# Performance work log

Measured on AMD Instinct MI355X. Metric: run time of the kernel, lower is better.

The kernel has to match this reference:

```python
import jax, jax.numpy as jnp
import numpy as np

N_OSC = 2          # oscillators per group
GROUPS = 64        # channels // n_oscillators
EPS_GN = 1e-5      # GroupNorm eps (torch default)
EPS_NORM = 1e-12   # F.normalize clamp (torch default)


def setup_inputs() -> dict:
    key = jax.random.key(0)
    k0, k1, k2 = jax.random.split(key, 3)
    B, C, H, W = 8, 128, 96, 96
    KS = 7
    return {
        "x": jax.random.normal(k0, (B, C, H, W), jnp.float32),
        "c": jax.random.normal(k1, (B, C, H, W), jnp.float32),
        "conv_w": jax.random.normal(k2, (C, C, KS, KS), jnp.float32) * 0.02,
        "conv_b": jnp.zeros((C,), jnp.float32),
        "gn_w": jnp.ones((C,), jnp.float32),
        "gn_b": jnp.zeros((C,), jnp.float32),
        "omega": jnp.ones((1,), jnp.float32),
        "n_timesteps": 4,
    }


def _group_norm(c, w, b):
    B, C, H, W = c.shape
    cg = c.reshape(B, GROUPS, C // GROUPS, H, W)
    mu = cg.mean(axis=(2, 3, 4), keepdims=True)
    var = ((cg - mu) ** 2).mean(axis=(2, 3, 4), keepdims=True)
    cg = (cg - mu) * jax.lax.rsqrt(var + EPS_GN)
    return cg.reshape(B, C, H, W) * w[None, :, None, None] + b[None, :, None, None]


def _normalize_osc(x):
    # L2-normalize each group of N_OSC channels (unit-norm oscillators)
    B, C, H, W = x.shape
    xg = x.reshape(B, C // N_OSC, N_OSC, H, W)
    n = jnp.sqrt((xg * xg).sum(axis=2, keepdims=True))
    xg = xg / jnp.maximum(n, EPS_NORM)
    return xg.reshape(B, C, H, W)


def _conv(x, w, b):
    y = jax.lax.conv_general_dilated(
        x, w, window_strides=(1, 1), padding=[(3, 3), (3, 3)],
        dimension_numbers=("NCHW", "OIHW", "NCHW"))
    return y + b[None, :, None, None]


def _kuramoto_step(x, coupling, stim, omega, gamma):
    B, C, H, W = x.shape
    G = C // N_OSC
    y = coupling + stim                      # total drive
    xg = x.reshape(B, G, N_OSC, H, W)
    yg = y.reshape(B, G, N_OSC, H, W)
    # natural-frequency term: rotate each 2D oscillator pair by omega
    xp = xg.reshape(B, G, N_OSC // 2, 2, H, W)
    rot = jnp.stack([-xp[:, :, :, 1], xp[:, :, :, 0]], axis=3)
    omega_term = omega * rot.reshape(B, G, N_OSC, H, W)
    # project drive onto tangent space of the unit sphere per group
    inner = (xg * yg).sum(axis=2, keepdims=True)
    proj = yg - inner * xg
    x_new = _normalize_osc((xg + gamma * (omega_term + proj)).reshape(B, C, H, W))
    energy = -(y * x).sum(axis=(1, 2, 3))    # per-sample Kuramoto energy
    return x_new, energy


def reference(x, c, conv_w, conv_b, gn_w, gn_b, omega, n_timesteps):
    gamma = 1.0
    B = x.shape[0]
    c = _group_norm(c, gn_w, gn_b)
    x = _normalize_osc(x)
    om = omega.squeeze()
    xs = []
    es = [jnp.zeros((B,), x.dtype)]
    for _ in range(int(n_timesteps)):
        coupling = _conv(x, conv_w, conv_b)
        x, e = _kuramoto_step(x, coupling, c, om, gamma)
        xs.append(x)
        es.append(e)
    return jnp.stack(xs), jnp.stack(es)
```

## Files before the change

### kernel.cpp

```cpp
#include <hip/hip_runtime.h>
#include <math.h>

typedef unsigned short u16;
typedef unsigned int   u32;
typedef unsigned char  u8;
typedef __attribute__((ext_vector_type(4))) float f32x4;
typedef __attribute__((ext_vector_type(4))) u32   u32x4;
typedef __attribute__((ext_vector_type(8))) int   i32x8;
typedef __attribute__((ext_vector_type(4))) int   i32x4;

#define IMG_W 96
#define IMG_H 96
#define HWSZ  9216
#define CCH   128
#define BATCH 8
#define NT    4

#define PADW  102
#define PADA  (102*102)
#define XQ_BYTES ((size_t)BATCH*PADA*128)

#define XS_ELEMS (BATCH*CCH*HWSZ)
#define ES_OFF   (4*XS_ELEMS)

__device__ inline u16 f2bf(float f) {
    u32 u = __float_as_uint(f);
    u += 0x7fffu + ((u >> 16) & 1u);
    return (u16)(u >> 16);
}
__device__ inline float bf2f(u16 h) { return __uint_as_float(((u32)h) << 16); }

#define GLD_LDS16(g, l) \
    __builtin_amdgcn_global_load_lds((const __attribute__((address_space(1))) void*)(g), \
                                     (__attribute__((address_space(3))) void*)(l), 16, 0, 0)

__global__ __launch_bounds__(256) void gn_stats_kernel(
    const float* __restrict__ c, float* __restrict__ stats)
{
    const int bg  = blockIdx.x;
    const int tid = threadIdx.x;
    const float4* p4 = (const float4*)(c + (size_t)bg * 18432);
    float s1 = 0.f, s2 = 0.f;
    for (int i = tid; i < 18432/4; i += 256) {
        float4 v = p4[i];
        s1 += v.x + v.y + v.z + v.w;
        s2 += v.x*v.x + v.y*v.y + v.z*v.z + v.w*v.w;
    }
    __shared__ float r1[256], r2[256];
    r1[tid] = s1; r2[tid] = s2;
    __syncthreads();
    for (int s = 128; s > 0; s >>= 1) {
        if (tid < s) { r1[tid] += r1[tid+s]; r2[tid] += r2[tid+s]; }
        __syncthreads();
    }
    if (tid == 0) {
        float mu  = r1[0] * (1.f/18432.f);
        float var = fmaxf(r2[0] * (1.f/18432.f) - mu*mu, 0.f);
        stats[bg*2]   = mu;
        stats[bg*2+1] = rsqrtf(var + 1e-5f);
    }
}

__global__ __launch_bounds__(256) void wprep_kernel(
    const float* __restrict__ cw, u32* __restrict__ wq)
{
    int idx = blockIdx.x * 256 + threadIdx.x;
    if (idx >= 200704) return;
    int ic4 = idx & 31;
    int rem = idx >> 5;
    int oc  = rem & 127;
    int tap = rem >> 7;
    const float* s = cw + ((size_t)oc*128 + ic4*4)*49 + tap;
    float v0 = s[0], v1 = s[49], v2 = s[98], v3 = s[147];
    u32 lo = __builtin_amdgcn_cvt_pk_fp8_f32(v0, v1, 0, false);
    u32 pk = __builtin_amdgcn_cvt_pk_fp8_f32(v2, v3, lo, true);
    wq[(size_t)tap*4096 + oc*32 + ic4] = pk;
}

__global__ __launch_bounds__(256) void cprep_kernel(
    const float* __restrict__ c, const float* __restrict__ stats,
    const float* __restrict__ gnw, const float* __restrict__ gnb,
    const float* __restrict__ cb, u32* __restrict__ cgn)
{
    const int bg  = blockIdx.y;
    const int pix = blockIdx.x * 1024 + threadIdx.x * 4;
    const int b   = bg >> 6, g = bg & 63;
    const int ch0 = 2*g, ch1 = 2*g + 1;
    const float mu = stats[bg*2], rs = stats[bg*2+1];
    const float w0 = gnw[ch0]*rs, b0 = gnb[ch0] - mu*w0 + cb[ch0];
    const float w1 = gnw[ch1]*rs, b1 = gnb[ch1] - mu*w1 + cb[ch1];
    f32x4 c0 = *(const f32x4*)(c + ((size_t)(b*128+ch0))*HWSZ + pix);
    f32x4 c1 = *(const f32x4*)(c + ((size_t)(b*128+ch1))*HWSZ + pix);
    u32x4 v;
    #pragma unroll
    for (int j = 0; j < 4; ++j)
        v[j] = (u32)f2bf(fmaf(c0[j], w0, b0)) | ((u32)f2bf(fmaf(c1[j], w1, b1)) << 16);
    *(u32x4*)(cgn + (size_t)bg*HWSZ + pix) = v;
}

__global__ __launch_bounds__(256) void xprep_kernel(
    const float* __restrict__ x, u8* __restrict__ xq)
{
    __shared__ float s_t[128][65];
    const int b  = blockIdx.y;
    const int p0 = blockIdx.x * 64;
    const int tid = threadIdx.x;
    for (int it = 0; it < 32; ++it) {
        int idx = it*256 + tid;
        int ch = idx >> 6, p = idx & 63;
        s_t[ch][p] = x[((size_t)b*128 + ch)*HWSZ + p0 + p];
    }
    __syncthreads();
    for (int it = 0; it < 16; ++it) {
        int idx = it*256 + tid;
        int g = idx & 63, p = idx >> 6;
        int pix = p0 + p;
        int py = pix / 96, px = pix - py*96;
        float v0 = s_t[2*g][p], v1 = s_t[2*g+1][p];
        float sc = 1.f / fmaxf(sqrtf(v0*v0 + v1*v1), 1e-12f);
        u32 pk = __builtin_amdgcn_cvt_pk_fp8_f32(v0*sc, v1*sc, 0, false);
        *(u16*)(xq + ((size_t)b*PADA + (py+3)*PADW + (px+3))*128 + 2*g) = (u16)(pk & 0xffff);
    }
}

__global__ __launch_bounds__(384, 3) void convk8(
    const u8*    __restrict__ xq_in,
    const u8*    __restrict__ wq,
    const u32*   __restrict__ cgn,
    const float* __restrict__ omega,
    float* __restrict__ xout, u8* __restrict__ xq_out,
    float* __restrict__ es, int write_q)
{
    __shared__ __align__(16) u8 s_a[324*128];
    __shared__ __align__(16) u8 s_bb[2][16384];
    __shared__ float s_red[384];

    const int tid = threadIdx.x;
    const int w   = tid >> 6, l = tid & 63;
    const int b   = blockIdx.y;
    const int bx  = blockIdx.x;
    const int tpy = bx >> 3, tpx = bx & 7;
    const int wm  = w >> 1, wn = w & 1;
    const int l15 = l & 15, l4 = l >> 4;

    const u8* abase = xq_in + ((size_t)b*PADA + (size_t)tpy*12*PADW + (size_t)tpx*12)*128;

#define BARX { __builtin_amdgcn_sched_barrier(0); __builtin_amdgcn_s_barrier(); \
               __builtin_amdgcn_sched_barrier(0); }
#define WAITV0 { asm volatile("s_waitcnt vmcnt(0)" ::: "memory"); \
                 __builtin_amdgcn_sched_barrier(0); }

    #pragma unroll 1
    for (int it = 0; it < 7; ++it) {
        int i = it*384 + tid;
        if (i < 2592) {
            int p = i >> 3, g = i & 7;
            int hr = p / 18, hc = p - hr*18;
            int sxy = (4*hr + hc) & 7;
            const u8* src = abase + ((size_t)hr*PADW + hc)*128 + ((g ^ sxy) << 4);
            GLD_LDS16(src, s_a + i*16);
        }
    }

#define ISSUE_B(ksrc, dstbuf)                                              \
    { const u8* wsrc_ = wq + (size_t)(ksrc)*16384;                         \
      _Pragma("unroll")                                                    \
      for (int it_ = 0; it_ < 3; ++it_) {                                  \
          int i_ = (it_*384 + tid) & 1023;                                 \
          int oc_ = i_ >> 3, g_ = i_ & 7;                                  \
          GLD_LDS16(wsrc_ + oc_*128 + ((g_ ^ (oc_ & 7)) << 4),             \
                    (dstbuf) + i_*16);                                     \
      } }

    ISSUE_B(0, s_bb[0]);
    WAITV0;
    BARX;

    int pb[3], sbz[3];
    #pragma unroll
    for (int mi = 0; mi < 3; ++mi) {
        int m = wm*48 + mi*16 + l15;
        int pr = m/12, pc = m - pr*12;
        pb[mi]  = pr*18 + pc;
        sbz[mi] = (4*pr + pc) & 7;
    }
    int boff[4];
    #pragma unroll
    for (int ni = 0; ni < 4; ++ni) {
        int oc = wn*64 + ni*16 + l15;
        boff[ni] = oc*128 + (((l4*2) ^ (oc & 7)) << 4);
    }
    const int kloA = (l4*2) << 4;

#define READ_FRAGS(AF, BF, sbuf)                                           \
    { _Pragma("unroll")                                                    \
      for (int mi_ = 0; mi_ < 3; ++mi_) {                                  \
          int plin_ = pb[mi_] + pdN;                                       \
          int sx_   = ((sbz[mi_] + sdN) & 7) << 4;                         \
          const u8* base_ = s_a + plin_*128;                               \
          int a0_ = kloA ^ sx_;                                            \
          i32x4 lo_ = *(const i32x4*)(base_ + a0_);                        \
          i32x4 hi_ = *(const i32x4*)(base_ + (a0_ ^ 16));                 \
          AF[mi_] = __builtin_shufflevector(lo_, hi_, 0,1,2,3,4,5,6,7);    \
      }                                                                    \
      _Pragma("unroll")                                                    \
      for (int ni_ = 0; ni_ < 4; ++ni_) {                                  \
          i32x4 lo_ = *(const i32x4*)((sbuf) + boff[ni_]);                 \
          i32x4 hi_ = *(const i32x4*)((sbuf) + (boff[ni_] ^ 16));          \
          BF[ni_] = __builtin_shufflevector(lo_, hi_, 0,1,2,3,4,5,6,7);    \
      } }

#define DO_MFMA(AF, BF)                                                    \
    __builtin_amdgcn_s_setprio(1);                                         \
    _Pragma("unroll")                                                      \
    for (int mi_ = 0; mi_ < 3; ++mi_)                                      \
        _Pragma("unroll")                                                  \
        for (int ni_ = 0; ni_ < 4; ++ni_)                                  \
            acc[mi_][ni_] = __builtin_amdgcn_mfma_scale_f32_16x16x128_f8f6f4( \
                BF[ni_], AF[mi_], acc[mi_][ni_], 0, 0, 0, 0x7F, 0, 0x7F);  \
    __builtin_amdgcn_s_setprio(0);

#define ADV { if (++txc == 7) { txc = 0; pdN += 12; sdN = (sdN + 6) & 7; } \
              else            { ++pdN;  sdN = (sdN + 1) & 7; } }

    f32x4 acc[3][4] = {};
    i32x8 af[3], bfr[4];
    int pdN = 0, sdN = 0, txc = 0;
    int cur = 0;

    #pragma unroll 1
    for (int t = 0; t < 48; ++t) {
        READ_FRAGS(af, bfr, s_bb[cur]);
        ADV;
        ISSUE_B(t+1, s_bb[cur^1]);
        DO_MFMA(af, bfr);
        WAITV0;
        BARX;
        cur ^= 1;
    }
    READ_FRAGS(af, bfr, s_bb[cur]);
    DO_MFMA(af, bfr);

    const float om = omega[0];
    const size_t nb = (size_t)b * (CCH*HWSZ);
    float esum = 0.f;

    #pragma unroll
    for (int mi = 0; mi < 3; ++mi) {
        const int m   = wm*48 + mi*16 + l15;
        const int pr  = m/12, pc = m - pr*12;
        const int py  = tpy*12 + pr;
        const int px  = tpx*12 + pc;
        const int pixel = py*96 + px;
        const int hp  = (pr+3)*18 + (pc+3);
        const int hs  = (4*(pr+3) + (pc+3)) & 7;
        const u8* albase = s_a + hp*128;
        #pragma unroll
        for (int ni = 0; ni < 4; ++ni) {
            const int ocb = wn*64 + ni*16 + l4*4;
            float res[4];
            #pragma unroll
            for (int p2 = 0; p2 < 2; ++p2) {
                const int oc0 = ocb + p2*2;
                const int g   = oc0 >> 1;
                int goff = (((oc0 >> 4) ^ hs) << 4) + (oc0 & 15);
                int xv   = (int)*(const u16*)(albase + goff);
                float x0 = __builtin_amdgcn_cvt_f32_fp8(xv, 0);
                float x1 = __builtin_amdgcn_cvt_f32_fp8(xv, 1);
                u32 cg = cgn[(size_t)(b*64 + g)*HWSZ + pixel];
                float y0 = acc[mi][ni][p2*2]   + bf2f((u16)(cg & 0xffff));
                float y1 = acc[mi][ni][p2*2+1] + bf2f((u16)(cg >> 16));
                float inner = x0*y0 + x1*y1;
                esum += inner;
                float xn0 = x0 - om*x1 + (y0 - inner*x0);
                float xn1 = x1 + om*x0 + (y1 - inner*x1);
                float sc2 = 1.f / fmaxf(sqrtf(xn0*xn0 + xn1*xn1), 1e-12f);
                res[p2*2]   = xn0 * sc2;
                res[p2*2+1] = xn1 * sc2;
                if (write_q) {
                    u32 pk = __builtin_amdgcn_cvt_pk_fp8_f32(res[p2*2], res[p2*2+1], 0, false);
                    *(u16*)(xq_out + ((size_t)b*PADA + (size_t)(py+3)*PADW + (px+3))*128 + oc0)
                        = (u16)(pk & 0xffff);
                }
            }
            #pragma unroll
            for (int j = 0; j < 4; ++j)
                xout[nb + (size_t)(ocb + j)*HWSZ + pixel] = res[j];
        }
    }

    s_red[tid] = esum;
    __syncthreads();
    if (tid < 128) s_red[tid] += s_red[tid+128] + s_red[tid+256];
    __syncthreads();
    for (int s = 64; s > 0; s >>= 1) {
        if (tid < s) s_red[tid] += s_red[tid+s];
        __syncthreads();
    }
    if (tid == 0) atomicAdd(es + b, -s_red[0]);
#undef ISSUE_B
#undef READ_FRAGS
#undef DO_MFMA
#undef ADV
#undef BARX
#undef WAITV0
}

template<bool FIRST>
__global__ __launch_bounds__(256) void conv_kur_kernel(
    const float* __restrict__ xin, const float* __restrict__ craw,
    const float* __restrict__ cw, const float* __restrict__ cb,
    const float* __restrict__ gnw, const float* __restrict__ gnb,
    const float* __restrict__ omega, const float* __restrict__ stats,
    float* __restrict__ xout, float* __restrict__ es)
{
    __shared__ float s_in[2][22][24];
    __shared__ float s_w[2][49][16];
    __shared__ float s_red[256];
    const int tid = threadIdx.x;
    const int tile = blockIdx.x, ocb = blockIdx.y, b = blockIdx.z;
    const int row0 = (tile / 6) * 16, col0 = (tile % 6) * 16;
    const int pxg = tid & 63, ocg = tid >> 6;
    const int ry = pxg >> 2, sx = pxg & 3;
    const size_t in_base = (size_t)b * CCH * HWSZ;
    float acc[4][4] = {};
    for (int icp = 0; icp < 64; ++icp) {
        __syncthreads();
        for (int idx = tid; idx < 968; idx += 256) {
            int ch = idx / 484, rem = idx - ch*484;
            int r = rem / 22, cl = rem - r*22;
            int gr = row0 + r - 3, gc = col0 + cl - 3;
            float v = 0.f;
            if (gr >= 0 && gr < IMG_H && gc >= 0 && gc < IMG_W)
                v = xin[in_base + (size_t)(icp*2 + ch)*HWSZ + gr*IMG_W + gc];
            s_in[ch][r][cl] = v;
        }
        {
            int combo = tid & 31, q = tid >> 5;
            if (q < 7) {
                int ch = combo >> 4, j = combo & 15;
                const float* wp = cw + ((size_t)(ocb*16 + j)*CCH + icp*2 + ch)*49 + q*7;
                #pragma unroll
                for (int t7 = 0; t7 < 7; ++t7) s_w[ch][q*7 + t7][j] = wp[t7];
            }
        }
        __syncthreads();
        if (FIRST) {
            for (int idx = tid; idx < 484; idx += 256) {
                int r = idx / 22, cl = idx - r*22;
                float v0 = s_in[0][r][cl], v1 = s_in[1][r][cl];
                float sc = 1.f / fmaxf(sqrtf(v0*v0 + v1*v1), 1e-12f);
                s_in[0][r][cl] = v0*sc; s_in[1][r][cl] = v1*sc;
            }
            __syncthreads();
        }
        #pragma unroll
        for (int ch = 0; ch < 2; ++ch)
            #pragma unroll
            for (int dy = 0; dy < 7; ++dy) {
                float r[12];
                const float* rp = &s_in[ch][ry + dy][sx*4];
                #pragma unroll
                for (int i = 0; i < 12; ++i) r[i] = rp[i];
                #pragma unroll
                for (int dx = 0; dx < 7; ++dx) {
                    const float* wv = &s_w[ch][dy*7 + dx][ocg*4];
                    float w0 = wv[0], w1 = wv[1], w2 = wv[2], w3 = wv[3];
                    #pragma unroll
                    for (int p = 0; p < 4; ++p) {
                        float iv = r[dx + p];
                        acc[0][p] = fmaf(w0, iv, acc[0][p]);
                        acc[1][p] = fmaf(w1, iv, acc[1][p]);
                        acc[2][p] = fmaf(w2, iv, acc[2][p]);
                        acc[3][p] = fmaf(w3, iv, acc[3][p]);
                    }
                }
            }
    }
    const int py = row0 + ry, px0 = col0 + sx*4;
    const float om = omega[0];
    const int ocbase = ocb*16 + ocg*4;
    float esum = 0.f;
    #pragma unroll
    for (int pr = 0; pr < 2; ++pr) {
        const int oc0 = ocbase + pr*2;
        const int g = oc0 >> 1;
        const float mu = stats[(b*64+g)*2], rs = stats[(b*64+g)*2+1];
        const float w0s = gnw[oc0]*rs,   b0s = gnb[oc0]   - mu*rs*gnw[oc0];
        const float w1s = gnw[oc0+1]*rs, b1s = gnb[oc0+1] - mu*rs*gnw[oc0+1];
        const float cb0 = cb[oc0], cb1 = cb[oc0+1];
        const size_t off = in_base + (size_t)oc0*HWSZ + py*IMG_W + px0;
        const float* c0p = craw + off; const float* c1p = c0p + HWSZ;
        const float* x0p = xin  + off; const float* x1p = x0p + HWSZ;
        float* o0p = xout + off; float* o1p = o0p + HWSZ;
        #pragma unroll
        for (int p = 0; p < 4; ++p) {
            float x0 = x0p[p], x1 = x1p[p];
            if (FIRST) {
                float sc = 1.f / fmaxf(sqrtf(x0*x0 + x1*x1), 1e-12f);
                x0 *= sc; x1 *= sc;
            }
            float y0 = acc[pr*2][p]   + cb0 + fmaf(c0p[p], w0s, b0s);
            float y1 = acc[pr*2+1][p] + cb1 + fmaf(c1p[p], w1s, b1s);
            float inner = x0*y0 + x1*y1;
            esum += inner;
            float xn0 = x0 - om*x1 + (y0 - inner*x0);
            float xn1 = x1 + om*x0 + (y1 - inner*x1);
            float sc2 = 1.f / fmaxf(sqrtf(xn0*xn0 + xn1*xn1), 1e-12f);
            o0p[p] = xn0*sc2; o1p[p] = xn1*sc2;
        }
    }
    s_red[tid] = esum;
    __syncthreads();
    for (int s = 128; s > 0; s >>= 1) {
        if (tid < s) s_red[tid] += s_red[tid + s];
        __syncthreads();
    }
    if (tid == 0) atomicAdd(es + b, -s_red[0]);
}

extern "C" void kernel_launch(void* const* d_in, const int* in_sizes, int n_in,
                              void* d_out, int out_size, void* d_ws, size_t ws_size,
                              hipStream_t stream)
{
    const float* x   = (const float*)d_in[0];
    const float* c   = (const float*)d_in[1];
    const float* cw  = (const float*)d_in[2];
    const float* cb  = (const float*)d_in[3];
    const float* gnw = (const float*)d_in[4];
    const float* gnb = (const float*)d_in[5];
    const float* om  = (const float*)d_in[6];
    float* out = (float*)d_out;

    float* stats = (float*)d_ws;
    hipMemsetAsync(out + ES_OFF, 0, 40 * sizeof(float), stream);
    gn_stats_kernel<<<512, 256, 0, stream>>>(c, stats);

    const size_t OFF_WQ  = 4096;
    const size_t OFF_CGN = OFF_WQ  + 802816;
    const size_t OFF_XQA = OFF_CGN + 18874368;
    const size_t OFF_XQB = OFF_XQA + XQ_BYTES;
    const size_t WS_NEED = OFF_XQB + XQ_BYTES;

    if (ws_size >= WS_NEED) {
        u32* wq   = (u32*)((char*)d_ws + OFF_WQ);
        u32* cgnp = (u32*)((char*)d_ws + OFF_CGN);
        u8*  xqA  = (u8*) ((char*)d_ws + OFF_XQA);
        u8*  xqB  = (u8*) ((char*)d_ws + OFF_XQB);

        hipMemsetAsync(xqA, 0, XQ_BYTES, stream);
        hipMemsetAsync(xqB, 0, XQ_BYTES, stream);
        wprep_kernel<<<(200704 + 255)/256, 256, 0, stream>>>(cw, wq);
        cprep_kernel<<<dim3(9, 512), 256, 0, stream>>>(c, stats, gnw, gnb, cb, cgnp);
        xprep_kernel<<<dim3(144, 8), 256, 0, stream>>>(x, xqA);

        dim3 grid(64, 8);
        u8* xin  = xqA;
        u8* xalt = xqB;
        for (int t = 0; t < NT; ++t) {
            float* xo  = out + (size_t)t * XS_ELEMS;
            float* esl = out + ES_OFF + (t + 1) * 8;
            int wb = (t < NT-1) ? 1 : 0;
            convk8<<<grid, 384, 0, stream>>>((const u8*)xin, (const u8*)wq, cgnp,
                                             om, xo, xalt, esl, wb);
            u8* tmp = xin; xin = xalt; xalt = tmp;
        }
    } else {
        dim3 grid(36, 8, 8);
        const float* xin = x;
        for (int t = 0; t < NT; ++t) {
            float* xo  = out + (size_t)t * XS_ELEMS;
            float* esl = out + ES_OFF + (t + 1) * 8;
            if (t == 0)
                conv_kur_kernel<true ><<<grid, 256, 0, stream>>>(xin, c, cw, cb, gnw, gnb, om, stats, xo, esl);
            else
                conv_kur_kernel<false><<<grid, 256, 0, stream>>>(xin, c, cw, cb, gnw, gnb, om, stats, xo, esl);
            xin = xo;
        }
    }
}
```

Before: 443.0 us.

## Double-buffer MFMA fragments in registers and unroll conv K-loop by two

The fp8 conv main loop is unrolled by two and gains two register sets of A/B fragments. The next step's fragments are read from LDS while the current step's MFMAs issue. The explicit vmcnt(0) wait plus raw s_barrier is replaced by __syncthreads, with the weight-tile prefetch issued right after each barrier. The aim is to hide LDS read latency behind MFMA work and loosen the per-step wait. In exchange it costs more VGPRs and relies on __syncthreads to order the async global-to-LDS loads.

```diff
diff --git a/kernel.cpp b/kernel.cpp
--- a/kernel.cpp
+++ b/kernel.cpp
@@ -145,11 +145,6 @@
 
     const u8* abase = xq_in + ((size_t)b*PADA + (size_t)tpy*12*PADW + (size_t)tpx*12)*128;
 
-#define BARX { __builtin_amdgcn_sched_barrier(0); __builtin_amdgcn_s_barrier(); \
-               __builtin_amdgcn_sched_barrier(0); }
-#define WAITV0 { asm volatile("s_waitcnt vmcnt(0)" ::: "memory"); \
-                 __builtin_amdgcn_sched_barrier(0); }
-
     #pragma unroll 1
     for (int it = 0; it < 7; ++it) {
         int i = it*384 + tid;
@@ -173,8 +168,7 @@
       } }
 
     ISSUE_B(0, s_bb[0]);
-    WAITV0;
-    BARX;
+    __syncthreads();
 
     int pb[3], sbz[3];
     #pragma unroll
@@ -224,22 +218,27 @@
               else            { ++pdN;  sdN = (sdN + 1) & 7; } }
 
     f32x4 acc[3][4] = {};
-    i32x8 af[3], bfr[4];
+    i32x8 af0[3], bf0r[4], af1[3], bf1r[4];
     int pdN = 0, sdN = 0, txc = 0;
-    int cur = 0;
+
+    READ_FRAGS(af0, bf0r, s_bb[0]);
+    ADV;
+    ISSUE_B(1, s_bb[1]);
 
     #pragma unroll 1
-    for (int t = 0; t < 48; ++t) {
-        READ_FRAGS(af, bfr, s_bb[cur]);
+    for (int t = 0; t < 48; t += 2) {
+        __syncthreads();
+        ISSUE_B(t+2, s_bb[0]);
+        READ_FRAGS(af1, bf1r, s_bb[1]);
         ADV;
-        ISSUE_B(t+1, s_bb[cur^1]);
-        DO_MFMA(af, bfr);
-        WAITV0;
-        BARX;
-        cur ^= 1;
-    }
-    READ_FRAGS(af, bfr, s_bb[cur]);
-    DO_MFMA(af, bfr);
+        DO_MFMA(af0, bf0r);
+        __syncthreads();
+        if (t + 3 < 49) ISSUE_B(t+3, s_bb[1]);
+        READ_FRAGS(af0, bf0r, s_bb[0]);
+        ADV;
+        DO_MFMA(af1, bf1r);
+    }
+    DO_MFMA(af0, bf0r);
 
     const float om = omega[0];
     const size_t nb = (size_t)b * (CCH*HWSZ);
@@ -302,8 +301,6 @@
 #undef READ_FRAGS
 #undef DO_MFMA
 #undef ADV
-#undef BARX
-#undef WAITV0
 }
 
 template<bool FIRST>
```

New measurement: 1.049 ms. 137% more time.
